# Performance work log

Measured on AMD Instinct MI355X. Metric: run time of the kernel, lower is better.

## Reference

```python
import jax, jax.numpy as jnp
import numpy as np

T, B, D = 2048, 256, 32
H0, H1, O = 64, 64, 35


def _fastgrnn_scan(xs, h0, W, U, bg, bu, zeta, nu):
    """Run FastGRNN recurrence. xs: [T, N, Din], h0: [N, H] -> hiddenStates [T, N, H].
    z = sigmoid(xW + hU + bg); c = tanh(xW + hU + bu);
    h = z*h + (sigmoid(zeta)*(1-z) + sigmoid(nu))*c
    """
    zs = jax.nn.sigmoid(zeta)  # [1,1]
    ns = jax.nn.sigmoid(nu)    # [1,1]
    xW = jnp.einsum('tnd,dh->tnh', xs, W)  # precompute input projections (same math)

    def step(h, xw):
        pre = xw + h @ U
        z = jax.nn.sigmoid(pre + bg)
        c = jnp.tanh(pre + bu)
        h_new = z * h + (zs * (1.0 - z) + ns) * c
        return h_new, h_new

    _, hs = jax.lax.scan(step, h0, xW)
    return hs


def setup_inputs() -> dict:
    key = jax.random.key(0)
    ks = jax.random.split(key, 8)
    x = jax.random.normal(ks[0], (T, B, D), dtype=jnp.float32)
    # FastGRNNCell params, layer 0 (inputDim -> hiddenDim0), full-rank (wRank=uRank=None)
    W0 = 0.1 * jax.random.normal(ks[1], (D, H0), dtype=jnp.float32)
    U0 = 0.1 * jax.random.normal(ks[2], (H0, H0), dtype=jnp.float32)
    bg0 = jnp.ones((1, H0), jnp.float32)
    bu0 = jnp.ones((1, H0), jnp.float32)
    zeta0 = 1.0 * jnp.ones((1, 1), jnp.float32)
    nu0 = -4.0 * jnp.ones((1, 1), jnp.float32)
    # layer 1 (hiddenDim0 -> hiddenDim1)
    W1 = 0.1 * jax.random.normal(ks[3], (H0, H1), dtype=jnp.float32)
    U1 = 0.1 * jax.random.normal(ks[4], (H1, H1), dtype=jnp.float32)
    bg1 = jnp.ones((1, H1), jnp.float32)
    bu1 = jnp.ones((1, H1), jnp.float32)
    zeta1 = 1.0 * jnp.ones((1, 1), jnp.float32)
    nu1 = -4.0 * jnp.ones((1, 1), jnp.float32)
    # output projection
    Wout = jax.random.normal(ks[5], (H1, O), dtype=jnp.float32)
    Bout = jax.random.normal(ks[6], (O,), dtype=jnp.float32)
    return {
        'x': x, 'brickSize': 32,
        'W0': W0, 'U0': U0, 'bg0': bg0, 'bu0': bu0, 'zeta0': zeta0, 'nu0': nu0,
        'W1': W1, 'U1': U1, 'bg1': bg1, 'bu1': bu1, 'zeta1': zeta1, 'nu1': nu1,
        'Wout': Wout, 'Bout': Bout,
    }


def reference(x, brickSize, W0, U0, bg0, bu0, zeta0, nu0,
              W1, U1, bg1, bu1, zeta1, nu1, Wout, Bout):
    t, b, d = x.shape
    numBricks = t // brickSize
    x = x[:numBricks * brickSize]
    # brick: [numBricks, brickSize, B, D] -> [brickSize, numBricks*B, D]
    xb = x.reshape(numBricks, brickSize, b, d)
    xb = jnp.transpose(xb, (1, 0, 2, 3)).reshape(brickSize, numBricks * b, d)
    # layer-0 FastGRNN over the brick time axis
    h0_init = jnp.zeros((numBricks * b, W0.shape[1]), x.dtype)
    hs0 = _fastgrnn_scan(xb, h0_init, W0, U0, bg0, bu0, zeta0, nu0)
    last0 = hs0[-1].reshape(numBricks, b, W0.shape[1])  # [numBricks, B, H0]
    # layer-1 FastGRNN over the brick axis
    h1_init = jnp.zeros((b, W1.shape[1]), x.dtype)
    hs1 = _fastgrnn_scan(last0, h1_init, W1, U1, bg1, bu1, zeta1, nu1)
    out = hs1[-1] @ Wout + Bout  # [B, outputDim]
    return out
```

## Files before the change

### kernel.cpp

```cpp
#include <hip/hip_runtime.h>
#include <hip/hip_bf16.h>


#define NB    64
#define BS    32
#define BATCH 256
#define D0    32
#define H     64
#define OUTD  35

typedef short  bf8   __attribute__((ext_vector_type(8)));
typedef float  f32x4 __attribute__((ext_vector_type(4)));

__device__ __forceinline__ float rcp_fast(float x) {
    return __builtin_amdgcn_rcpf(x);
}
__device__ __forceinline__ float sigm(float x) {
    return rcp_fast(1.0f + __expf(-x));
}
__device__ __forceinline__ float tanh_safe(float x) {
    float a = fabsf(x);
    float e = __expf(-2.0f * a);
    float m = (1.0f - e) * rcp_fast(1.0f + e);
    return copysignf(m, x);
}
__device__ __forceinline__ short f2bf(float f) {
    __hip_bfloat16 b = __float2bfloat16(f);
    return __builtin_bit_cast(short, b);
}

__global__ __launch_bounds__(256, 4) void l0_kernel(
    const float* __restrict__ x,
    const float* __restrict__ W,
    const float* __restrict__ U,
    const float* __restrict__ bg,
    const float* __restrict__ bu,
    const float* __restrict__ zeta,
    const float* __restrict__ nu,
    float* __restrict__ last0)
{
    __shared__ unsigned char hb[2][16 * 128];

    const int tid  = threadIdx.x;
    const int lane = tid & 63;
    const int wn   = __builtin_amdgcn_readfirstlane(tid >> 6);
    const int l15  = lane & 15;
    const int lg   = lane >> 4;

    const int brick     = blockIdx.x >> 4;
    const int batchbase = (blockIdx.x & 15) << 4;

    *reinterpret_cast<float2*>(&hb[0][tid * 8]) = make_float2(0.f, 0.f);

    bf8 Wb, Ub0, Ub1;
    const int ucol = wn * 16 + l15;
#pragma unroll
    for (int j = 0; j < 8; ++j) Wb[j]  = f2bf(W[(8 * lg + j) * H + ucol]);
#pragma unroll
    for (int j = 0; j < 8; ++j) Ub0[j] = f2bf(U[(8 * lg + j) * H + ucol]);
#pragma unroll
    for (int j = 0; j < 8; ++j) Ub1[j] = f2bf(U[(32 + 8 * lg + j) * H + ucol]);

    const float bgc = bg[ucol], buc = bu[ucol];
    const float zs  = sigm(zeta[0]);
    const float ns  = sigm(nu[0]);

    float hc[4] = {0.f, 0.f, 0.f, 0.f};

    const float* xbase = x + ((size_t)(brick * BS) * BATCH + batchbase + l15) * D0 + 8 * lg;
    const size_t xstep = (size_t)BATCH * D0;

    float4 xa0 = reinterpret_cast<const float4*>(xbase)[0];
    float4 xa1 = reinterpret_cast<const float4*>(xbase)[1];
    float4 xn0 = reinterpret_cast<const float4*>(xbase + xstep)[0];
    float4 xn1 = reinterpret_cast<const float4*>(xbase + xstep)[1];

    __syncthreads();

    int cur = 0;
#pragma unroll 1
    for (int t = 0; t < BS; ++t) {
        const int tp = (t + 2 < BS) ? (t + 2) : (BS - 1);
        float4 p0 = reinterpret_cast<const float4*>(xbase + (size_t)tp * xstep)[0];
        float4 p1 = reinterpret_cast<const float4*>(xbase + (size_t)tp * xstep)[1];

        bf8 xa;
        xa[0] = f2bf(xa0.x); xa[1] = f2bf(xa0.y); xa[2] = f2bf(xa0.z); xa[3] = f2bf(xa0.w);
        xa[4] = f2bf(xa1.x); xa[5] = f2bf(xa1.y); xa[6] = f2bf(xa1.z); xa[7] = f2bf(xa1.w);

        f32x4 acc = {0.f, 0.f, 0.f, 0.f};
        acc = __builtin_amdgcn_mfma_f32_16x16x32_bf16(xa, Wb, acc, 0, 0, 0);

        const unsigned char* hr = &hb[cur][l15 * 128];
        const int swz = (l15 & 7) << 4;
        bf8 ha0 = *reinterpret_cast<const bf8*>(hr + ((16 * lg) ^ swz));
        bf8 ha1 = *reinterpret_cast<const bf8*>(hr + ((64 + 16 * lg) ^ swz));
        acc = __builtin_amdgcn_mfma_f32_16x16x32_bf16(ha0, Ub0, acc, 0, 0, 0);
        acc = __builtin_amdgcn_mfma_f32_16x16x32_bf16(ha1, Ub1, acc, 0, 0, 0);

#pragma unroll
        for (int r = 0; r < 4; ++r) {
            float pre = acc[r];
            float z = sigm(pre + bgc);
            float c = tanh_safe(pre + buc);
            hc[r] = z * hc[r] + (zs * (1.f - z) + ns) * c;
        }

        {
            unsigned char* wb = &hb[cur ^ 1][0];
#pragma unroll
            for (int r = 0; r < 4; ++r) {
                int s   = 4 * lg + r;
                int off = s * 128 + ((ucol * 2) ^ ((s & 7) << 4));
                *reinterpret_cast<short*>(wb + off) = f2bf(hc[r]);
            }
        }
        __syncthreads();
        cur ^= 1;
        xa0 = xn0; xa1 = xn1;
        xn0 = p0;  xn1 = p1;
    }

    {
        float* op = last0 + ((size_t)(brick * BATCH + batchbase)) * H;
#pragma unroll
        for (int r = 0; r < 4; ++r) {
            int s = 4 * lg + r;
            op[(size_t)s * H + ucol] = hc[r];
        }
    }
}

__global__ __launch_bounds__(256, 1) void l1_kernel(
    const float* __restrict__ last0,
    const float* __restrict__ W,
    const float* __restrict__ U,
    const float* __restrict__ bg,
    const float* __restrict__ bu,
    const float* __restrict__ zeta,
    const float* __restrict__ nu,
    const float* __restrict__ Wout,
    const float* __restrict__ Bout,
    float* __restrict__ out)
{
    __shared__ float px[NB][H];
    __shared__ float hbb[H];

    const int lane  = threadIdx.x & 63;
    const int wave  = __builtin_amdgcn_readfirstlane(threadIdx.x >> 6);
    const int batch = blockIdx.x;

    float wc[H];
#pragma unroll
    for (int k = 0; k < H; ++k) wc[k] = W[k * H + lane];

#pragma unroll 1
    for (int t = wave * 16; t < wave * 16 + 16; ++t) {
        const float* ip = last0 + ((size_t)(t * BATCH + batch)) * H;
        float a0 = 0.f, a1 = 0.f, a2 = 0.f, a3 = 0.f;
#pragma unroll
        for (int q = 0; q < H / 4; ++q) {
            a0 = fmaf(ip[4 * q + 0], wc[4 * q + 0], a0);
            a1 = fmaf(ip[4 * q + 1], wc[4 * q + 1], a1);
            a2 = fmaf(ip[4 * q + 2], wc[4 * q + 2], a2);
            a3 = fmaf(ip[4 * q + 3], wc[4 * q + 3], a3);
        }
        px[t][lane] = (a0 + a1) + (a2 + a3);
    }
    __syncthreads();
    if (wave != 0) return;

    float uc[H];
#pragma unroll
    for (int k = 0; k < H; ++k) uc[k] = U[k * H + lane];

    const float zs  = sigm(zeta[0]);
    const float ns  = sigm(nu[0]);
    const float bgj = bg[lane];
    const float buj = bu[lane];

    float h = 0.f;
    hbb[lane] = 0.f;

#pragma unroll 1
    for (int t = 0; t < NB; ++t) {
        float a0 = px[t][lane], a1 = 0.f, a2 = 0.f, a3 = 0.f;
#pragma unroll
        for (int q = 0; q < H / 4; ++q) {
            float4 hv = *reinterpret_cast<const float4*>(&hbb[4 * q]);
            a0 = fmaf(hv.x, uc[4 * q + 0], a0);
            a1 = fmaf(hv.y, uc[4 * q + 1], a1);
            a2 = fmaf(hv.z, uc[4 * q + 2], a2);
            a3 = fmaf(hv.w, uc[4 * q + 3], a3);
        }
        float a = (a0 + a1) + (a2 + a3);
        float z = sigm(a + bgj);
        float c = tanh_safe(a + buj);
        h = z * h + (zs * (1.f - z) + ns) * c;
        hbb[lane] = h;
    }

    if (lane < OUTD) {
        float o = Bout[lane];
#pragma unroll
        for (int k = 0; k < H; ++k) o = fmaf(hbb[k], Wout[k * OUTD + lane], o);
        out[batch * OUTD + lane] = o;
    }
}

extern "C" void kernel_launch(void* const* d_in, const int* in_sizes, int n_in,
                              void* d_out, int out_size, void* d_ws, size_t ws_size,
                              hipStream_t stream) {
    const float* x    = (const float*)d_in[0];
    const float* W0   = (const float*)d_in[2];
    const float* U0   = (const float*)d_in[3];
    const float* bg0  = (const float*)d_in[4];
    const float* bu0  = (const float*)d_in[5];
    const float* z0   = (const float*)d_in[6];
    const float* n0   = (const float*)d_in[7];
    const float* W1   = (const float*)d_in[8];
    const float* U1   = (const float*)d_in[9];
    const float* bg1  = (const float*)d_in[10];
    const float* bu1  = (const float*)d_in[11];
    const float* z1   = (const float*)d_in[12];
    const float* n1   = (const float*)d_in[13];
    const float* Wout = (const float*)d_in[14];
    const float* Bout = (const float*)d_in[15];
    float* out = (float*)d_out;

    float* last0 = (float*)d_ws;

    l0_kernel<<<1024, 256, 0, stream>>>(x, W0, U0, bg0, bu0, z0, n0, last0);
    l1_kernel<<<BATCH, 256, 0, stream>>>(last0, W1, U1, bg1, bu1, z1, n1, Wout, Bout, out);
}
```

Measured before the change: 72.95 us.

## Rewrite layer-1 recurrence with bf16 MFMA over 16-batch tiles, streamline gates

The layer-1 kernel moves from one block per batch element, with scalar FMA input projection and a single-wave serial recurrence, to 16 blocks that each handle 16 batch rows. Each step uses bf16 MFMA for both the input and hidden projections, with a swizzled LDS double buffer and register prefetch of the layer-0 states two steps ahead. Both kernels also switch to a cheaper tanh formula, packed bf16 conversions and a refactored gate update. The risks are fewer blocks, meaning low parallelism across the 64 serial steps, bf16 precision on the layer-1 path, and possible overflow or precision loss in the simplified tanh for large inputs.

```diff
diff --git a/kernel.cpp b/kernel.cpp
--- a/kernel.cpp
+++ b/kernel.cpp
@@ -18,16 +18,22 @@
 __device__ __forceinline__ float sigm(float x) {
     return rcp_fast(1.0f + __expf(-x));
 }
-__device__ __forceinline__ float tanh_safe(float x) {
-    float a = fabsf(x);
-    float e = __expf(-2.0f * a);
-    float m = (1.0f - e) * rcp_fast(1.0f + e);
-    return copysignf(m, x);
+__device__ __forceinline__ float tanh_fast(float x) {
+    float q = rcp_fast(1.0f + __expf(-2.0f * x));
+    return fmaf(2.0f, q, -1.0f);
 }
 __device__ __forceinline__ short f2bf(float f) {
     __hip_bfloat16 b = __float2bfloat16(f);
     return __builtin_bit_cast(short, b);
 }
+__device__ __forceinline__ unsigned pk2bf(float lo, float hi) {
+    __hip_bfloat162 h2 = __float22bfloat162_rn(make_float2(lo, hi));
+    unsigned r;
+    __builtin_memcpy(&r, &h2, 4);
+    return r;
+}
+
+union U4BF8 { unsigned u[4]; bf8 v; };
 
 __global__ __launch_bounds__(256, 4) void l0_kernel(
     const float* __restrict__ x,
@@ -64,6 +70,7 @@
     const float bgc = bg[ucol], buc = bu[ucol];
     const float zs  = sigm(zeta[0]);
     const float ns  = sigm(nu[0]);
+    const float zns = zs + ns;
 
     float hc[4] = {0.f, 0.f, 0.f, 0.f};
 
@@ -74,6 +81,14 @@
     float4 xa1 = reinterpret_cast<const float4*>(xbase)[1];
     float4 xn0 = reinterpret_cast<const float4*>(xbase + xstep)[0];
     float4 xn1 = reinterpret_cast<const float4*>(xbase + xstep)[1];
+
+    int woff[4];
+#pragma unroll
+    for (int r = 0; r < 4; ++r) {
+        int s = 4 * lg + r;
+        woff[r] = s * 128 + ((ucol * 2) ^ ((s & 7) << 4));
+    }
+    const int swz = (l15 & 7) << 4;
 
     __syncthreads();
 
@@ -84,15 +99,16 @@
         float4 p0 = reinterpret_cast<const float4*>(xbase + (size_t)tp * xstep)[0];
         float4 p1 = reinterpret_cast<const float4*>(xbase + (size_t)tp * xstep)[1];
 
-        bf8 xa;
-        xa[0] = f2bf(xa0.x); xa[1] = f2bf(xa0.y); xa[2] = f2bf(xa0.z); xa[3] = f2bf(xa0.w);
-        xa[4] = f2bf(xa1.x); xa[5] = f2bf(xa1.y); xa[6] = f2bf(xa1.z); xa[7] = f2bf(xa1.w);
+        U4BF8 xp;
+        xp.u[0] = pk2bf(xa0.x, xa0.y);
+        xp.u[1] = pk2bf(xa0.z, xa0.w);
+        xp.u[2] = pk2bf(xa1.x, xa1.y);
+        xp.u[3] = pk2bf(xa1.z, xa1.w);
 
         f32x4 acc = {0.f, 0.f, 0.f, 0.f};
-        acc = __builtin_amdgcn_mfma_f32_16x16x32_bf16(xa, Wb, acc, 0, 0, 0);
+        acc = __builtin_amdgcn_mfma_f32_16x16x32_bf16(xp.v, Wb, acc, 0, 0, 0);
 
         const unsigned char* hr = &hb[cur][l15 * 128];
-        const int swz = (l15 & 7) << 4;
         bf8 ha0 = *reinterpret_cast<const bf8*>(hr + ((16 * lg) ^ swz));
         bf8 ha1 = *reinterpret_cast<const bf8*>(hr + ((64 + 16 * lg) ^ swz));
         acc = __builtin_amdgcn_mfma_f32_16x16x32_bf16(ha0, Ub0, acc, 0, 0, 0);
@@ -100,20 +116,20 @@
 
 #pragma unroll
         for (int r = 0; r < 4; ++r) {
-            float pre = acc[r];
-            float z = sigm(pre + bgc);
-            float c = tanh_safe(pre + buc);
-            hc[r] = z * hc[r] + (zs * (1.f - z) + ns) * c;
+            float z = sigm(acc[r] + bgc);
+            float c = tanh_fast(acc[r] + buc);
+            float w = fmaf(-zs, z, zns);
+            hc[r] = fmaf(z, hc[r], w * c);
         }
 
         {
             unsigned char* wb = &hb[cur ^ 1][0];
-#pragma unroll
-            for (int r = 0; r < 4; ++r) {
-                int s   = 4 * lg + r;
-                int off = s * 128 + ((ucol * 2) ^ ((s & 7) << 4));
-                *reinterpret_cast<short*>(wb + off) = f2bf(hc[r]);
-            }
+            unsigned pk01 = pk2bf(hc[0], hc[1]);
+            unsigned pk23 = pk2bf(hc[2], hc[3]);
+            *reinterpret_cast<unsigned short*>(wb + woff[0]) = (unsigned short)pk01;
+            *reinterpret_cast<unsigned short*>(wb + woff[1]) = (unsigned short)(pk01 >> 16);
+            *reinterpret_cast<unsigned short*>(wb + woff[2]) = (unsigned short)pk23;
+            *reinterpret_cast<unsigned short*>(wb + woff[3]) = (unsigned short)(pk23 >> 16);
         }
         __syncthreads();
         cur ^= 1;
@@ -143,68 +159,122 @@
     const float* __restrict__ Bout,
     float* __restrict__ out)
 {
-    __shared__ float px[NB][H];
-    __shared__ float hbb[H];
-
-    const int lane  = threadIdx.x & 63;
-    const int wave  = __builtin_amdgcn_readfirstlane(threadIdx.x >> 6);
-    const int batch = blockIdx.x;
-
-    float wc[H];
-#pragma unroll
-    for (int k = 0; k < H; ++k) wc[k] = W[k * H + lane];
-
-#pragma unroll 1
-    for (int t = wave * 16; t < wave * 16 + 16; ++t) {
-        const float* ip = last0 + ((size_t)(t * BATCH + batch)) * H;
-        float a0 = 0.f, a1 = 0.f, a2 = 0.f, a3 = 0.f;
-#pragma unroll
-        for (int q = 0; q < H / 4; ++q) {
-            a0 = fmaf(ip[4 * q + 0], wc[4 * q + 0], a0);
-            a1 = fmaf(ip[4 * q + 1], wc[4 * q + 1], a1);
-            a2 = fmaf(ip[4 * q + 2], wc[4 * q + 2], a2);
-            a3 = fmaf(ip[4 * q + 3], wc[4 * q + 3], a3);
-        }
-        px[t][lane] = (a0 + a1) + (a2 + a3);
-    }
-    __syncthreads();
-    if (wave != 0) return;
-
-    float uc[H];
-#pragma unroll
-    for (int k = 0; k < H; ++k) uc[k] = U[k * H + lane];
-
+    __shared__ unsigned char hb[2][16 * 128];
+    __shared__ float hsf[16][H];
+
+    const int tid  = threadIdx.x;
+    const int lane = tid & 63;
+    const int wn   = __builtin_amdgcn_readfirstlane(tid >> 6);
+    const int l15  = lane & 15;
+    const int lg   = lane >> 4;
+
+    const int batchbase = blockIdx.x << 4;
+
+    *reinterpret_cast<float2*>(&hb[0][tid * 8]) = make_float2(0.f, 0.f);
+
+    bf8 Wb0, Wb1, Ub0, Ub1;
+    const int ucol = wn * 16 + l15;
+#pragma unroll
+    for (int j = 0; j < 8; ++j) Wb0[j] = f2bf(W[(8 * lg + j) * H + ucol]);
+#pragma unroll
+    for (int j = 0; j < 8; ++j) Wb1[j] = f2bf(W[(32 + 8 * lg + j) * H + ucol]);
+#pragma unroll
+    for (int j = 0; j < 8; ++j) Ub0[j] = f2bf(U[(8 * lg + j) * H + ucol]);
+#pragma unroll
+    for (int j = 0; j < 8; ++j) Ub1[j] = f2bf(U[(32 + 8 * lg + j) * H + ucol]);
+
+    const float bgc = bg[ucol], buc = bu[ucol];
     const float zs  = sigm(zeta[0]);
     const float ns  = sigm(nu[0]);
-    const float bgj = bg[lane];
-    const float buj = bu[lane];
-
-    float h = 0.f;
-    hbb[lane] = 0.f;
-
+    const float zns = zs + ns;
+
+    float hc[4] = {0.f, 0.f, 0.f, 0.f};
+
+    const float* abase = last0 + ((size_t)(batchbase + l15)) * H + 8 * lg;
+    const size_t astep = (size_t)BATCH * H;
+
+    float4 cA0 = reinterpret_cast<const float4*>(abase)[0];
+    float4 cA1 = reinterpret_cast<const float4*>(abase)[1];
+    float4 cA2 = reinterpret_cast<const float4*>(abase + 32)[0];
+    float4 cA3 = reinterpret_cast<const float4*>(abase + 32)[1];
+    float4 nA0 = reinterpret_cast<const float4*>(abase + astep)[0];
+    float4 nA1 = reinterpret_cast<const float4*>(abase + astep)[1];
+    float4 nA2 = reinterpret_cast<const float4*>(abase + astep + 32)[0];
+    float4 nA3 = reinterpret_cast<const float4*>(abase + astep + 32)[1];
+
+    int woff[4];
+#pragma unroll
+    for (int r = 0; r < 4; ++r) {
+        int s = 4 * lg + r;
+        woff[r] = s * 128 + ((ucol * 2) ^ ((s & 7) << 4));
+    }
+    const int swz = (l15 & 7) << 4;
+
+    __syncthreads();
+
+    int cur = 0;
 #pragma unroll 1
     for (int t = 0; t < NB; ++t) {
-        float a0 = px[t][lane], a1 = 0.f, a2 = 0.f, a3 = 0.f;
-#pragma unroll
-        for (int q = 0; q < H / 4; ++q) {
-            float4 hv = *reinterpret_cast<const float4*>(&hbb[4 * q]);
-            a0 = fmaf(hv.x, uc[4 * q + 0], a0);
-            a1 = fmaf(hv.y, uc[4 * q + 1], a1);
-            a2 = fmaf(hv.z, uc[4 * q + 2], a2);
-            a3 = fmaf(hv.w, uc[4 * q + 3], a3);
-        }
-        float a = (a0 + a1) + (a2 + a3);
-        float z = sigm(a + bgj);
-        float c = tanh_safe(a + buj);
-        h = z * h + (zs * (1.f - z) + ns) * c;
-        hbb[lane] = h;
-    }
-
-    if (lane < OUTD) {
-        float o = Bout[lane];
-#pragma unroll
-        for (int k = 0; k < H; ++k) o = fmaf(hbb[k], Wout[k * OUTD + lane], o);
-        out[batch * OUTD + lane] = o;
+        const int tp = (t + 2 < NB) ? (t + 2) : (NB - 1);
+        float4 p0 = reinterpret_cast<const float4*>(abase + (size_t)tp * astep)[0];
+        float4 p1 = reinterpret_cast<const float4*>(abase + (size_t)tp * astep)[1];
+        float4 p2 = reinterpret_cast<const float4*>(abase + (size_t)tp * astep + 32)[0];
+        float4 p3 = reinterpret_cast<const float4*>(abase + (size_t)tp * astep + 32)[1];
+
+        U4BF8 a0, a1;
+        a0.u[0] = pk2bf(cA0.x, cA0.y);
+        a0.u[1] = pk2bf(cA0.z, cA0.w);
+        a0.u[2] = pk2bf(cA1.x, cA1.y);
+        a0.u[3] = pk2bf(cA1.z, cA1.w);
+        a1.u[0] = pk2bf(cA2.x, cA2.y);
+        a1.u[1] = pk2bf(cA2.z, cA2.w);
+        a1.u[2] = pk2bf(cA3.x, cA3.y);
+        a1.u[3] = pk2bf(cA3.z, cA3.w);
+
+        f32x4 acc = {0.f, 0.f, 0.f, 0.f};
+        acc = __builtin_amdgcn_mfma_f32_16x16x32_bf16(a0.v, Wb0, acc, 0, 0, 0);
+        acc = __builtin_amdgcn_mfma_f32_16x16x32_bf16(a1.v, Wb1, acc, 0, 0, 0);
+
+        const unsigned char* hr = &hb[cur][l15 * 128];
+        bf8 ha0 = *reinterpret_cast<const bf8*>(hr + ((16 * lg) ^ swz));
+        bf8 ha1 = *reinterpret_cast<const bf8*>(hr + ((64 + 16 * lg) ^ swz));
+        acc = __builtin_amdgcn_mfma_f32_16x16x32_bf16(ha0, Ub0, acc, 0, 0, 0);
+        acc = __builtin_amdgcn_mfma_f32_16x16x32_bf16(ha1, Ub1, acc, 0, 0, 0);
+
+#pragma unroll
+        for (int r = 0; r < 4; ++r) {
+            float z = sigm(acc[r] + bgc);
+            float c = tanh_fast(acc[r] + buc);
+            float w = fmaf(-zs, z, zns);
+            hc[r] = fmaf(z, hc[r], w * c);
+        }
+
+        {
+            unsigned char* wb = &hb[cur ^ 1][0];
+            unsigned pk01 = pk2bf(hc[0], hc[1]);
+            unsigned pk23 = pk2bf(hc[2], hc[3]);
+            *reinterpret_cast<unsigned short*>(wb + woff[0]) = (unsigned short)pk01;
+            *reinterpret_cast<unsigned short*>(wb + woff[1]) = (unsigned short)(pk01 >> 16);
+            *reinterpret_cast<unsigned short*>(wb + woff[2]) = (unsigned short)pk23;
+            *reinterpret_cast<unsigned short*>(wb + woff[3]) = (unsigned short)(pk23 >> 16);
+        }
+        __syncthreads();
+        cur ^= 1;
+        cA0 = nA0; cA1 = nA1; cA2 = nA2; cA3 = nA3;
+        nA0 = p0;  nA1 = p1;  nA2 = p2;  nA3 = p3;
+    }
+
+#pragma unroll
+    for (int r = 0; r < 4; ++r) hsf[4 * lg + r][ucol] = hc[r];
+    __syncthreads();
+
+    for (int p = tid; p < 16 * OUTD; p += 256) {
+        int s = p / OUTD;
+        int o = p - s * OUTD;
+        float a = Bout[o];
+#pragma unroll
+        for (int u = 0; u < H; ++u) a = fmaf(hsf[s][u], Wout[u * OUTD + o], a);
+        out[(size_t)(batchbase + s) * OUTD + o] = a;
     }
 }
 
@@ -231,5 +301,5 @@
     float* last0 = (float*)d_ws;
 
     l0_kernel<<<1024, 256, 0, stream>>>(x, W0, U0, bg0, bu0, z0, n0, last0);
-    l1_kernel<<<BATCH, 256, 0, stream>>>(last0, W1, U1, bg1, bu1, z1, n1, Wout, Bout, out);
-}
+    l1_kernel<<<16, 256, 0, stream>>>(last0, W1, U1, bg1, bu1, z1, n1, Wout, Bout, out);
+}
```

Result: slower. 94.90 us (+30.1%).
